# Performance work log

Hardware: AMD Instinct MI355X
Metric: run time of the kernel (lower is better)

Reference implementation:

```python
import jax, jax.numpy as jnp
import numpy as np

D_MODEL = 1024
N_HEADS = 16
D_K = D_MODEL // N_HEADS


def _xavier(key, shape):
    fan_in, fan_out = shape[1], shape[0]
    a = np.sqrt(6.0 / (fan_in + fan_out))
    return jax.random.uniform(key, shape, jnp.float32, -a, a)


def setup_inputs() -> dict:
    key = jax.random.key(0)
    kx, kq, kk, kv, ko = jax.random.split(key, 5)
    x = jax.random.normal(kx, (2, 2048, D_MODEL), jnp.float32)
    # nn.Linear weights are [out, in]; y = x @ W.T
    Wq = _xavier(kq, (D_MODEL, D_MODEL))
    Wk = _xavier(kk, (D_MODEL, D_MODEL))
    Wv = _xavier(kv, (D_MODEL, D_MODEL))
    Wo = _xavier(ko, (D_MODEL, D_MODEL))
    bo = jnp.zeros((D_MODEL,), jnp.float32)
    return {"x": x, "Wq": Wq, "Wk": Wk, "Wv": Wv, "Wo": Wo, "bo": bo}


def reference(x, Wq, Wk, Wv, Wo, bo):
    B, S, D = x.shape
    def split_heads(t):
        # [B,S,D] -> [B,H,S,d_k]
        return t.reshape(B, S, N_HEADS, D_K).transpose(0, 2, 1, 3)
    Q = split_heads(x @ Wq.T)
    K = split_heads(x @ Wk.T)
    V = split_heads(x @ Wv.T)
    scale = 1.0 / jnp.sqrt(jnp.asarray(D_K, x.dtype))
    scores = jnp.einsum('bhqd,bhkd->bhqk', Q, K) * scale  # [B,H,S,S]
    attn = jax.nn.softmax(scores, axis=-1)
    out = jnp.einsum('bhqk,bhkd->bhqd', attn, V)  # [B,H,S,d_k]
    out = out.transpose(0, 2, 1, 3).reshape(B, S, D)  # merge heads
    return out @ Wo.T + bo
```

## Files before the change

### kernel.cpp

```cpp
#include <hip/hip_runtime.h>


typedef __attribute__((ext_vector_type(8))) short bf16x8;
typedef __attribute__((ext_vector_type(4))) short bf16x4;
typedef __attribute__((ext_vector_type(4))) float f32x4;
typedef __attribute__((ext_vector_type(2))) unsigned int u32x2;

#define GK 1024
#define SEQ 2048
#define NHEAD 16
#define DKD 64
#define PADW 72

#define MFMA32(a, b, c) __builtin_amdgcn_mfma_f32_16x16x32_bf16((a), (b), (c), 0, 0, 0)
#define MFMA16(a, b, c) __builtin_amdgcn_mfma_f32_16x16x16bf16_1k((a), (b), (c), 0, 0, 0)

#if __has_builtin(__builtin_amdgcn_exp2f)
#define EXP2(x) __builtin_amdgcn_exp2f(x)
#else
#define EXP2(x) exp2f(x)
#endif

#define QSCALE 0.18033688011f

static __device__ __forceinline__ unsigned short f2bf(float f) {
    unsigned int u = __float_as_uint(f);
    u += 0x7fffu + ((u >> 16) & 1u);
    return (unsigned short)(u >> 16);
}

static __device__ __forceinline__ unsigned int pack_bf2(float a, float b) {
    unsigned int ua = __float_as_uint(a) + 0x8000u;
    unsigned int ub = __float_as_uint(b) + 0x8000u;
    return __builtin_amdgcn_perm(ub, ua, 0x07060302u);
}

__global__ __launch_bounds__(256) void cast_all(const float* __restrict__ x,
                                                const float* __restrict__ wq,
                                                const float* __restrict__ wk,
                                                const float* __restrict__ wv,
                                                const float* __restrict__ wo,
                                                unsigned short* __restrict__ Xb,
                                                unsigned short* __restrict__ Wqkv,
                                                unsigned short* __restrict__ Wob) {
    const int bid = blockIdx.x;
    const float* src; unsigned short* dst; int off;
    if (bid < 4096)      { src = x;  dst = Xb;             off = bid; }
    else if (bid < 5120) { src = wq; dst = Wqkv;           off = bid - 4096; }
    else if (bid < 6144) { src = wk; dst = Wqkv + 1048576; off = bid - 5120; }
    else if (bid < 7168) { src = wv; dst = Wqkv + 2097152; off = bid - 6144; }
    else                 { src = wo; dst = Wob;            off = bid - 7168; }
    const int i = off * 1024 + threadIdx.x * 4;
    float4 v = *(const float4*)(src + i);
    u32x2 p; p.x = pack_bf2(v.x, v.y); p.y = pack_bf2(v.z, v.w);
    *(u32x2*)(dst + i) = p;
}

template <int MODE, int BN>
__global__ __launch_bounds__(256) void gemm_bt(const unsigned short* __restrict__ A,
                                               const unsigned short* __restrict__ Bw,
                                               unsigned short* __restrict__ outb,
                                               float* __restrict__ outf,
                                               const float* __restrict__ bias) {
    constexpr int NJ = BN / 32;
    constexpr int LOOP_BYTES = 128 * 64 * 2 + BN * 64 * 2;
    constexpr int EPI_BYTES  = 4 * 64 * PADW * 2;
    constexpr int SMEM_BYTES = (MODE == 0)
        ? (LOOP_BYTES > EPI_BYTES ? LOOP_BYTES : EPI_BYTES)
        : LOOP_BYTES;
    __shared__ __align__(16) unsigned char SMEM[SMEM_BYTES];
    unsigned short* As = (unsigned short*)SMEM;
    unsigned short* Bs = As + 128 * 64;

    const int t    = threadIdx.x;
    const int lane = t & 63;
    const int w    = t >> 6;
    const int wm   = (w >> 1) * 64;
    const int wn   = (w & 1) * (BN / 2);
    const int bm0  = blockIdx.x * 128;
    const int bn0  = blockIdx.y * BN;
    const int lm   = lane & 15;
    const int lq   = lane >> 4;
    const int swzb = lm & 7;

    const unsigned short* Ab = A + (size_t)bm0 * GK;
    const unsigned short* Bb = Bw + (size_t)bn0 * GK;

    f32x4 acc[4][NJ];
    const f32x4 Z4 = {0.f, 0.f, 0.f, 0.f};
#pragma unroll
    for (int i = 0; i < 4; i++)
#pragma unroll
        for (int j = 0; j < NJ; j++) acc[i][j] = Z4;

    const int q_uni = (t & ~63);

    for (int k0 = 0; k0 < GK; k0 += 64) {
        __syncthreads();
#pragma unroll
        for (int i = 0; i < 4; ++i) {
            int q  = i * 256 + t;
            int r  = q >> 3;
            int gc = (q & 7) ^ (r & 7);
            int q0 = i * 256 + q_uni;
            __builtin_amdgcn_global_load_lds(
                (const __attribute__((address_space(1))) void*)(Ab + (size_t)r * GK + k0 + gc * 8),
                (__attribute__((address_space(3))) void*)(As + (size_t)q0 * 8),
                16, 0, 0);
        }
#pragma unroll
        for (int i = 0; i < BN / 32; ++i) {
            int q  = i * 256 + t;
            int r  = q >> 3;
            int gc = (q & 7) ^ (r & 7);
            int q0 = i * 256 + q_uni;
            __builtin_amdgcn_global_load_lds(
                (const __attribute__((address_space(1))) void*)(Bb + (size_t)r * GK + k0 + gc * 8),
                (__attribute__((address_space(3))) void*)(Bs + (size_t)q0 * 8),
                16, 0, 0);
        }
        __syncthreads();

#pragma unroll
        for (int kk = 0; kk < 2; ++kk) {
            const int swz = ((kk * 4 + lq) ^ swzb) * 8;
            bf16x8 af[4], bf[NJ];
#pragma unroll
            for (int i = 0; i < 4; i++)
                af[i] = *(const bf16x8*)(As + (wm + i * 16 + lm) * 64 + swz);
#pragma unroll
            for (int j = 0; j < NJ; j++)
                bf[j] = *(const bf16x8*)(Bs + (wn + j * 16 + lm) * 64 + swz);
#pragma unroll
            for (int i = 0; i < 4; i++)
#pragma unroll
                for (int j = 0; j < NJ; j++)
                    acc[i][j] = MFMA32(af[i], bf[j], acc[i][j]);
        }
    }

    if (MODE == 0) {
        __syncthreads();
        unsigned short* E  = (unsigned short*)SMEM;
        unsigned short* Ew = E + w * (64 * PADW);
        const int nbase = bn0 + wn;
        const int which = nbase >> 10;
        const int hh    = (nbase & 1023) >> 6;
        if (which != 2) {
            const float sc = (which == 0) ? QSCALE : 1.0f;
#pragma unroll
            for (int i = 0; i < 4; i++)
#pragma unroll
                for (int j = 0; j < 4; j++)
#pragma unroll
                    for (int r = 0; r < 4; r++)
                        Ew[(i * 16 + lq * 4 + r) * PADW + j * 16 + lm] =
                            f2bf(acc[i][j][r] * sc);
            unsigned short* dst = outb + (size_t)which * 4194304;
#pragma unroll
            for (int rep = 0; rep < 8; ++rep) {
                const int mm = rep * 8 + (lane >> 3);
                const int d0 = (lane & 7) * 8;
                uint4 v = *(const uint4*)(Ew + mm * PADW + d0);
                const int m_g = bm0 + wm + mm;
                const int b = m_g >> 11, s = m_g & 2047;
                *(uint4*)(dst + (((size_t)(b * NHEAD + hh)) * SEQ + s) * DKD + d0) = v;
            }
        } else {
#pragma unroll
            for (int i = 0; i < 4; i++)
#pragma unroll
                for (int j = 0; j < 4; j++) {
                    u32x2 pk;
                    pk.x = pack_bf2(acc[i][j][0], acc[i][j][1]);
                    pk.y = pack_bf2(acc[i][j][2], acc[i][j][3]);
                    *(u32x2*)(Ew + (j * 16 + lm) * PADW + i * 16 + lq * 4) = pk;
                }
            unsigned short* dst = outb + (size_t)2 * 4194304;
#pragma unroll
            for (int rep = 0; rep < 8; ++rep) {
                const int nn = rep * 8 + (lane >> 3);
                const int mc = (lane & 7) * 8;
                uint4 v = *(const uint4*)(Ew + nn * PADW + mc);
                const int m_g = bm0 + wm + mc;
                const int b = m_g >> 11, s0 = m_g & 2047;
                *(uint4*)(dst + (((size_t)(b * NHEAD + hh)) * DKD + nn) * SEQ + s0) = v;
            }
        }
    } else {
#pragma unroll
        for (int i = 0; i < 4; i++) {
            const int mbase = bm0 + wm + i * 16 + lq * 4;
#pragma unroll
            for (int j = 0; j < NJ; j++) {
                const int n = bn0 + wn + j * 16 + lm;
#pragma unroll
                for (int r = 0; r < 4; r++)
                    outf[(size_t)(mbase + r) * 1024 + n] = acc[i][j][r] + bias[n];
            }
        }
    }
}

__global__ __launch_bounds__(256, 3) void attn_kernel(const unsigned short* __restrict__ Qg,
                                                      const unsigned short* __restrict__ Kg,
                                                      const unsigned short* __restrict__ Vtg,
                                                      unsigned short* __restrict__ Og) {
    __shared__ __align__(16) unsigned short KV[2][2][64 * PADW];

    const int id  = blockIdx.x;
    const int xcd = id & 7;
    const int j8  = id >> 3;
    const int bh  = xcd * 4 + (j8 & 3);
    const int qb  = j8 >> 2;
    const unsigned short* Qp  = Qg  + ((size_t)bh * SEQ + qb * 64) * DKD;
    const unsigned short* Kp  = Kg  + (size_t)bh * SEQ * DKD;
    const unsigned short* Vtp = Vtg + (size_t)bh * DKD * SEQ;

    const int t    = threadIdx.x;
    const int lane = t & 63;
    const int w    = t >> 6;
    const int lm   = lane & 15;
    const int kq   = lane >> 4;

    const f32x4 Z4 = {0.f, 0.f, 0.f, 0.f};

    bf16x8 aq[4][2];
#pragma unroll
    for (int c = 0; c < 4; ++c)
#pragma unroll
        for (int kk = 0; kk < 2; ++kk)
            aq[c][kk] = *(const bf16x8*)(Qp + (size_t)(c * 16 + lm) * DKD + kk * 32 + kq * 8);

    f32x4 o[4][4];
    float ls[4];
#pragma unroll
    for (int c = 0; c < 4; ++c) {
        ls[c] = 0.f;
#pragma unroll
        for (int dj = 0; dj < 4; ++dj) o[c][dj] = Z4;
    }

    const int sr = t >> 2, sc = (t & 3) * 16;
    uint4 kreg0, kreg1, vreg0, vreg1;
    {
        const unsigned short* kp = Kp + (size_t)sr * DKD + sc;
        const unsigned short* vp = Vtp + (size_t)sr * SEQ + sc;
        uint4 a0 = *(const uint4*)(kp), a1 = *(const uint4*)(kp + 8);
        uint4 b0 = *(const uint4*)(vp), b1 = *(const uint4*)(vp + 8);
        uint4* dk = (uint4*)(&KV[0][0][sr * PADW + sc]); dk[0] = a0; dk[1] = a1;
        uint4* dv = (uint4*)(&KV[0][1][sr * PADW + sc]); dv[0] = b0; dv[1] = b1;
    }
    {
        const unsigned short* kp = Kp + (size_t)(64 + sr) * DKD + sc;
        kreg0 = *(const uint4*)(kp); kreg1 = *(const uint4*)(kp + 8);
        const unsigned short* vp = Vtp + (size_t)sr * SEQ + 64 + sc;
        vreg0 = *(const uint4*)(vp); vreg1 = *(const uint4*)(vp + 8);
    }

    for (int kt = 0; kt < 32; ++kt) {
        __syncthreads();
        if (kt + 1 < 32) {
            uint4* dk = (uint4*)(&KV[(kt + 1) & 1][0][sr * PADW + sc]);
            dk[0] = kreg0; dk[1] = kreg1;
            uint4* dv = (uint4*)(&KV[(kt + 1) & 1][1][sr * PADW + sc]);
            dv[0] = vreg0; dv[1] = vreg1;
        }
        if (kt + 2 < 32) {
            const unsigned short* kp = Kp + (size_t)((kt + 2) * 64 + sr) * DKD + sc;
            kreg0 = *(const uint4*)(kp); kreg1 = *(const uint4*)(kp + 8);
            const unsigned short* vp = Vtp + (size_t)sr * SEQ + (kt + 2) * 64 + sc;
            vreg0 = *(const uint4*)(vp); vreg1 = *(const uint4*)(vp + 8);
        }
        const unsigned short* Kc = &KV[kt & 1][0][0];
        const unsigned short* Vc = &KV[kt & 1][1][0];

        bf16x8 ak0 = *(const bf16x8*)(Kc + (w * 16 + lm) * PADW + kq * 8);
        bf16x8 ak1 = *(const bf16x8*)(Kc + (w * 16 + lm) * PADW + 32 + kq * 8);
        f32x4 s[4];
#pragma unroll
        for (int c = 0; c < 4; ++c) {
            s[c] = MFMA32(ak0, aq[c][0], Z4);
            s[c] = MFMA32(ak1, aq[c][1], s[c]);
        }

#pragma unroll
        for (int c = 0; c < 4; ++c) {
#pragma unroll
            for (int r = 0; r < 4; ++r) s[c][r] = EXP2(s[c][r]);
            ls[c] += (s[c][0] + s[c][1]) + (s[c][2] + s[c][3]);
        }

        bf16x4 ap[4];
#pragma unroll
        for (int c = 0; c < 4; ++c) {
            u32x2 pk;
            pk.x = pack_bf2(s[c][0], s[c][1]);
            pk.y = pack_bf2(s[c][2], s[c][3]);
            ap[c] = __builtin_bit_cast(bf16x4, pk);
        }

#pragma unroll
        for (int dj = 0; dj < 4; ++dj) {
            bf16x4 bv = *(const bf16x4*)(Vc + (dj * 16 + lm) * PADW + w * 16 + kq * 4);
#pragma unroll
            for (int c = 0; c < 4; ++c)
                o[c][dj] = MFMA16(ap[c], bv, o[c][dj]);
        }
    }

    __syncthreads();
    float* Lf = (float*)(&KV[0][0][0]);

#pragma unroll
    for (int c = 0; c < 4; ++c) {
        float v = ls[c];
        v += __shfl_xor(v, 16);
        v += __shfl_xor(v, 32);
        if (kq == 0) Lf[w * 64 + c * 16 + lm] = v;
    }
    __syncthreads();

    const int rq = t >> 2;
    const int dq = (t & 3) * 8;
    float li = (Lf[rq] + Lf[64 + rq]) + (Lf[128 + rq] + Lf[192 + rq]);
#if __has_builtin(__builtin_amdgcn_rcpf)
    li = __builtin_amdgcn_rcpf(li);
#else
    li = 1.0f / li;
#endif
    __syncthreads();

    const int b = bh >> 4, h = bh & 15;
#pragma unroll
    for (int p = 0; p < 2; ++p) {
#pragma unroll
        for (int c = 0; c < 4; ++c)
#pragma unroll
            for (int djh = 0; djh < 2; ++djh) {
                const int dj = 2 * p + djh;
#pragma unroll
                for (int r = 0; r < 4; ++r)
                    Lf[(w * 64 + c * 16 + kq * 4 + r) * 36 + djh * 16 + lm] = o[c][dj][r];
            }
        __syncthreads();
        f32x4 a0 = Z4, a1 = Z4;
#pragma unroll
        for (int wp = 0; wp < 4; ++wp) {
            a0 += *(const f32x4*)(Lf + (wp * 64 + rq) * 36 + dq);
            a1 += *(const f32x4*)(Lf + (wp * 64 + rq) * 36 + dq + 4);
        }
        uint4 outv;
        outv.x = pack_bf2(a0[0] * li, a0[1] * li);
        outv.y = pack_bf2(a0[2] * li, a0[3] * li);
        outv.z = pack_bf2(a1[0] * li, a1[1] * li);
        outv.w = pack_bf2(a1[2] * li, a1[3] * li);
        *(uint4*)(Og + (((size_t)(b * SEQ + qb * 64 + rq)) * NHEAD + h) * DKD + p * 32 + dq) = outv;
        __syncthreads();
    }
}

extern "C" void kernel_launch(void* const* d_in, const int* in_sizes, int n_in,
                              void* d_out, int out_size, void* d_ws, size_t ws_size,
                              hipStream_t stream) {
    const float* x  = (const float*)d_in[0];
    const float* Wq = (const float*)d_in[1];
    const float* Wk = (const float*)d_in[2];
    const float* Wv = (const float*)d_in[3];
    const float* Wo = (const float*)d_in[4];
    const float* bo = (const float*)d_in[5];
    float* out = (float*)d_out;

    unsigned short* ws = (unsigned short*)d_ws;
    unsigned short* Xb   = ws;
    unsigned short* Wqkv = ws + 4194304;
    unsigned short* Wob  = ws + 7340032;
    unsigned short* QKV  = ws + 8388608;
    unsigned short* Ob   = ws + 20971520;

    cast_all<<<8192, 256, 0, stream>>>(x, Wq, Wk, Wv, Wo, Xb, Wqkv, Wob);
    gemm_bt<0, 128><<<dim3(32, 24), 256, 0, stream>>>(Xb, Wqkv, QKV, nullptr, nullptr);
    attn_kernel<<<1024, 256, 0, stream>>>(QKV, QKV + 4194304, QKV + 8388608, Ob);
    gemm_bt<1, 64><<<dim3(32, 16), 256, 0, stream>>>(Ob, Wob, nullptr, out, bo);
}
```

Measured before the change: 190.5 us.

## Fuse fp32-to-bf16 cast of x into QKV GEMM with register prefetch

The separate cast of the activation x to bf16 is removed. The QKV GEMM now reads fp32 x directly, converts it to bf16 in registers, and stages it into LDS. Loading switches from async global_load_lds to register-prefetched loads for the next k-tile, which overlap with the MFMA work on the current tile. This removes a full write and re-read of the bf16 copy of x and one kernel's worth of blocks, but doubles the global bytes read for A per GEMM tile (re-read across 24 column blocks) and adds register pressure.

```diff
diff --git a/kernel.cpp b/kernel.cpp
--- a/kernel.cpp
+++ b/kernel.cpp
@@ -35,39 +35,30 @@
     return __builtin_amdgcn_perm(ub, ua, 0x07060302u);
 }
 
-__global__ __launch_bounds__(256) void cast_all(const float* __restrict__ x,
-                                                const float* __restrict__ wq,
-                                                const float* __restrict__ wk,
-                                                const float* __restrict__ wv,
-                                                const float* __restrict__ wo,
-                                                unsigned short* __restrict__ Xb,
-                                                unsigned short* __restrict__ Wqkv,
-                                                unsigned short* __restrict__ Wob) {
+__global__ __launch_bounds__(256) void cast_w(const float* __restrict__ wq,
+                                              const float* __restrict__ wk,
+                                              const float* __restrict__ wv,
+                                              const float* __restrict__ wo,
+                                              unsigned short* __restrict__ Wqkv,
+                                              unsigned short* __restrict__ Wob) {
     const int bid = blockIdx.x;
     const float* src; unsigned short* dst; int off;
-    if (bid < 4096)      { src = x;  dst = Xb;             off = bid; }
-    else if (bid < 5120) { src = wq; dst = Wqkv;           off = bid - 4096; }
-    else if (bid < 6144) { src = wk; dst = Wqkv + 1048576; off = bid - 5120; }
-    else if (bid < 7168) { src = wv; dst = Wqkv + 2097152; off = bid - 6144; }
-    else                 { src = wo; dst = Wob;            off = bid - 7168; }
+    if (bid < 1024)      { src = wq; dst = Wqkv;           off = bid; }
+    else if (bid < 2048) { src = wk; dst = Wqkv + 1048576; off = bid - 1024; }
+    else if (bid < 3072) { src = wv; dst = Wqkv + 2097152; off = bid - 2048; }
+    else                 { src = wo; dst = Wob;            off = bid - 3072; }
     const int i = off * 1024 + threadIdx.x * 4;
     float4 v = *(const float4*)(src + i);
     u32x2 p; p.x = pack_bf2(v.x, v.y); p.y = pack_bf2(v.z, v.w);
     *(u32x2*)(dst + i) = p;
 }
 
-template <int MODE, int BN>
-__global__ __launch_bounds__(256) void gemm_bt(const unsigned short* __restrict__ A,
-                                               const unsigned short* __restrict__ Bw,
-                                               unsigned short* __restrict__ outb,
-                                               float* __restrict__ outf,
-                                               const float* __restrict__ bias) {
-    constexpr int NJ = BN / 32;
-    constexpr int LOOP_BYTES = 128 * 64 * 2 + BN * 64 * 2;
+__global__ __launch_bounds__(256) void gemm_qkv(const float* __restrict__ X,
+                                                const unsigned short* __restrict__ Bw,
+                                                unsigned short* __restrict__ outb) {
+    constexpr int LOOP_BYTES = 128 * 64 * 2 * 2;
     constexpr int EPI_BYTES  = 4 * 64 * PADW * 2;
-    constexpr int SMEM_BYTES = (MODE == 0)
-        ? (LOOP_BYTES > EPI_BYTES ? LOOP_BYTES : EPI_BYTES)
-        : LOOP_BYTES;
+    constexpr int SMEM_BYTES = LOOP_BYTES > EPI_BYTES ? LOOP_BYTES : EPI_BYTES;
     __shared__ __align__(16) unsigned char SMEM[SMEM_BYTES];
     unsigned short* As = (unsigned short*)SMEM;
     unsigned short* Bs = As + 128 * 64;
@@ -76,22 +67,150 @@
     const int lane = t & 63;
     const int w    = t >> 6;
     const int wm   = (w >> 1) * 64;
-    const int wn   = (w & 1) * (BN / 2);
+    const int wn   = (w & 1) * 64;
     const int bm0  = blockIdx.x * 128;
-    const int bn0  = blockIdx.y * BN;
+    const int bn0  = blockIdx.y * 128;
     const int lm   = lane & 15;
     const int lq   = lane >> 4;
     const int swzb = lm & 7;
 
+    const int srow = t >> 3;
+    const int gc   = (t & 7) ^ (srow & 7);
+    const float*           Xa = X  + (size_t)(bm0 + srow) * GK + gc * 8;
+    const unsigned short*  Bb = Bw + (size_t)(bn0 + srow) * GK + gc * 8;
+
+    f32x4 acc[4][4];
+    const f32x4 Z4 = {0.f, 0.f, 0.f, 0.f};
+#pragma unroll
+    for (int i = 0; i < 4; i++)
+#pragma unroll
+        for (int j = 0; j < 4; j++) acc[i][j] = Z4;
+
+    uint4 pa[4], pb[4];
+#pragma unroll
+    for (int i = 0; i < 4; ++i) {
+        const float* xp = Xa + (size_t)i * 32 * GK;
+        float4 f0 = *(const float4*)(xp);
+        float4 f1 = *(const float4*)(xp + 4);
+        pa[i].x = pack_bf2(f0.x, f0.y); pa[i].y = pack_bf2(f0.z, f0.w);
+        pa[i].z = pack_bf2(f1.x, f1.y); pa[i].w = pack_bf2(f1.z, f1.w);
+        pb[i] = *(const uint4*)(Bb + (size_t)i * 32 * GK);
+    }
+
+    for (int kt = 0; kt < 16; ++kt) {
+        __syncthreads();
+#pragma unroll
+        for (int i = 0; i < 4; ++i) {
+            *(uint4*)(As + (size_t)(i * 256 + t) * 8) = pa[i];
+            *(uint4*)(Bs + (size_t)(i * 256 + t) * 8) = pb[i];
+        }
+        __syncthreads();
+        if (kt + 1 < 16) {
+            const int k0 = (kt + 1) * 64;
+#pragma unroll
+            for (int i = 0; i < 4; ++i) {
+                const float* xp = Xa + (size_t)i * 32 * GK + k0;
+                float4 f0 = *(const float4*)(xp);
+                float4 f1 = *(const float4*)(xp + 4);
+                pa[i].x = pack_bf2(f0.x, f0.y); pa[i].y = pack_bf2(f0.z, f0.w);
+                pa[i].z = pack_bf2(f1.x, f1.y); pa[i].w = pack_bf2(f1.z, f1.w);
+                pb[i] = *(const uint4*)(Bb + (size_t)i * 32 * GK + k0);
+            }
+        }
+#pragma unroll
+        for (int kk = 0; kk < 2; ++kk) {
+            const int swz = ((kk * 4 + lq) ^ swzb) * 8;
+            bf16x8 af[4], bf[4];
+#pragma unroll
+            for (int i = 0; i < 4; i++)
+                af[i] = *(const bf16x8*)(As + (wm + i * 16 + lm) * 64 + swz);
+#pragma unroll
+            for (int j = 0; j < 4; j++)
+                bf[j] = *(const bf16x8*)(Bs + (wn + j * 16 + lm) * 64 + swz);
+#pragma unroll
+            for (int i = 0; i < 4; i++)
+#pragma unroll
+                for (int j = 0; j < 4; j++)
+                    acc[i][j] = MFMA32(af[i], bf[j], acc[i][j]);
+        }
+    }
+
+    __syncthreads();
+    unsigned short* E  = (unsigned short*)SMEM;
+    unsigned short* Ew = E + w * (64 * PADW);
+    const int nbase = bn0 + wn;
+    const int which = nbase >> 10;
+    const int hh    = (nbase & 1023) >> 6;
+    if (which != 2) {
+        const float sc = (which == 0) ? QSCALE : 1.0f;
+#pragma unroll
+        for (int i = 0; i < 4; i++)
+#pragma unroll
+            for (int j = 0; j < 4; j++)
+#pragma unroll
+                for (int r = 0; r < 4; r++)
+                    Ew[(i * 16 + lq * 4 + r) * PADW + j * 16 + lm] =
+                        f2bf(acc[i][j][r] * sc);
+        unsigned short* dst = outb + (size_t)which * 4194304;
+#pragma unroll
+        for (int rep = 0; rep < 8; ++rep) {
+            const int mm = rep * 8 + (lane >> 3);
+            const int d0 = (lane & 7) * 8;
+            uint4 v = *(const uint4*)(Ew + mm * PADW + d0);
+            const int m_g = bm0 + wm + mm;
+            const int b = m_g >> 11, s = m_g & 2047;
+            *(uint4*)(dst + (((size_t)(b * NHEAD + hh)) * SEQ + s) * DKD + d0) = v;
+        }
+    } else {
+#pragma unroll
+        for (int i = 0; i < 4; i++)
+#pragma unroll
+            for (int j = 0; j < 4; j++) {
+                u32x2 pk;
+                pk.x = pack_bf2(acc[i][j][0], acc[i][j][1]);
+                pk.y = pack_bf2(acc[i][j][2], acc[i][j][3]);
+                *(u32x2*)(Ew + (j * 16 + lm) * PADW + i * 16 + lq * 4) = pk;
+            }
+        unsigned short* dst = outb + (size_t)2 * 4194304;
+#pragma unroll
+        for (int rep = 0; rep < 8; ++rep) {
+            const int nn = rep * 8 + (lane >> 3);
+            const int mc = (lane & 7) * 8;
+            uint4 v = *(const uint4*)(Ew + nn * PADW + mc);
+            const int m_g = bm0 + wm + mc;
+            const int b = m_g >> 11, s0 = m_g & 2047;
+            *(uint4*)(dst + (((size_t)(b * NHEAD + hh)) * DKD + nn) * SEQ + s0) = v;
+        }
+    }
+}
+
+__global__ __launch_bounds__(256) void gemm_proj(const unsigned short* __restrict__ A,
+                                                 const unsigned short* __restrict__ Bw,
+                                                 float* __restrict__ outf,
+                                                 const float* __restrict__ bias) {
+    __shared__ __align__(16) unsigned short As[128 * 64];
+    __shared__ __align__(16) unsigned short Bs[64 * 64];
+
+    const int t    = threadIdx.x;
+    const int lane = t & 63;
+    const int w    = t >> 6;
+    const int wm   = (w >> 1) * 64;
+    const int wn   = (w & 1) * 32;
+    const int bm0  = blockIdx.x * 128;
+    const int bn0  = blockIdx.y * 64;
+    const int lm   = lane & 15;
+    const int lq   = lane >> 4;
+    const int swzb = lm & 7;
+
     const unsigned short* Ab = A + (size_t)bm0 * GK;
     const unsigned short* Bb = Bw + (size_t)bn0 * GK;
 
-    f32x4 acc[4][NJ];
+    f32x4 acc[4][2];
     const f32x4 Z4 = {0.f, 0.f, 0.f, 0.f};
 #pragma unroll
     for (int i = 0; i < 4; i++)
 #pragma unroll
-        for (int j = 0; j < NJ; j++) acc[i][j] = Z4;
+        for (int j = 0; j < 2; j++) acc[i][j] = Z4;
 
     const int q_uni = (t & ~63);
 
@@ -99,23 +218,23 @@
         __syncthreads();
 #pragma unroll
         for (int i = 0; i < 4; ++i) {
-            int q  = i * 256 + t;
-            int r  = q >> 3;
-            int gc = (q & 7) ^ (r & 7);
-            int q0 = i * 256 + q_uni;
+            int q   = i * 256 + t;
+            int r   = q >> 3;
+            int gcs = (q & 7) ^ (r & 7);
+            int q0  = i * 256 + q_uni;
             __builtin_amdgcn_global_load_lds(
-                (const __attribute__((address_space(1))) void*)(Ab + (size_t)r * GK + k0 + gc * 8),
+                (const __attribute__((address_space(1))) void*)(Ab + (size_t)r * GK + k0 + gcs * 8),
                 (__attribute__((address_space(3))) void*)(As + (size_t)q0 * 8),
                 16, 0, 0);
         }
 #pragma unroll
-        for (int i = 0; i < BN / 32; ++i) {
-            int q  = i * 256 + t;
-            int r  = q >> 3;
-            int gc = (q & 7) ^ (r & 7);
-            int q0 = i * 256 + q_uni;
+        for (int i = 0; i < 2; ++i) {
+            int q   = i * 256 + t;
+            int r   = q >> 3;
+            int gcs = (q & 7) ^ (r & 7);
+            int q0  = i * 256 + q_uni;
             __builtin_amdgcn_global_load_lds(
-                (const __attribute__((address_space(1))) void*)(Bb + (size_t)r * GK + k0 + gc * 8),
+                (const __attribute__((address_space(1))) void*)(Bb + (size_t)r * GK + k0 + gcs * 8),
                 (__attribute__((address_space(3))) void*)(Bs + (size_t)q0 * 8),
                 16, 0, 0);
         }
@@ -124,80 +243,30 @@
 #pragma unroll
         for (int kk = 0; kk < 2; ++kk) {
             const int swz = ((kk * 4 + lq) ^ swzb) * 8;
-            bf16x8 af[4], bf[NJ];
+            bf16x8 af[4], bf[2];
 #pragma unroll
             for (int i = 0; i < 4; i++)
                 af[i] = *(const bf16x8*)(As + (wm + i * 16 + lm) * 64 + swz);
 #pragma unroll
-            for (int j = 0; j < NJ; j++)
+            for (int j = 0; j < 2; j++)
                 bf[j] = *(const bf16x8*)(Bs + (wn + j * 16 + lm) * 64 + swz);
 #pragma unroll
             for (int i = 0; i < 4; i++)
 #pragma unroll
-                for (int j = 0; j < NJ; j++)
+                for (int j = 0; j < 2; j++)
                     acc[i][j] = MFMA32(af[i], bf[j], acc[i][j]);
         }
     }
 
-    if (MODE == 0) {
-        __syncthreads();
-        unsigned short* E  = (unsigned short*)SMEM;
-        unsigned short* Ew = E + w * (64 * PADW);
-        const int nbase = bn0 + wn;
-        const int which = nbase >> 10;
-        const int hh    = (nbase & 1023) >> 6;
-        if (which != 2) {
-            const float sc = (which == 0) ? QSCALE : 1.0f;
-#pragma unroll
-            for (int i = 0; i < 4; i++)
-#pragma unroll
-                for (int j = 0; j < 4; j++)
-#pragma unroll
-                    for (int r = 0; r < 4; r++)
-                        Ew[(i * 16 + lq * 4 + r) * PADW + j * 16 + lm] =
-                            f2bf(acc[i][j][r] * sc);
-            unsigned short* dst = outb + (size_t)which * 4194304;
-#pragma unroll
-            for (int rep = 0; rep < 8; ++rep) {
-                const int mm = rep * 8 + (lane >> 3);
-                const int d0 = (lane & 7) * 8;
-                uint4 v = *(const uint4*)(Ew + mm * PADW + d0);
-                const int m_g = bm0 + wm + mm;
-                const int b = m_g >> 11, s = m_g & 2047;
-                *(uint4*)(dst + (((size_t)(b * NHEAD + hh)) * SEQ + s) * DKD + d0) = v;
-            }
-        } else {
-#pragma unroll
-            for (int i = 0; i < 4; i++)
-#pragma unroll
-                for (int j = 0; j < 4; j++) {
-                    u32x2 pk;
-                    pk.x = pack_bf2(acc[i][j][0], acc[i][j][1]);
-                    pk.y = pack_bf2(acc[i][j][2], acc[i][j][3]);
-                    *(u32x2*)(Ew + (j * 16 + lm) * PADW + i * 16 + lq * 4) = pk;
-                }
-            unsigned short* dst = outb + (size_t)2 * 4194304;
-#pragma unroll
-            for (int rep = 0; rep < 8; ++rep) {
-                const int nn = rep * 8 + (lane >> 3);
-                const int mc = (lane & 7) * 8;
-                uint4 v = *(const uint4*)(Ew + nn * PADW + mc);
-                const int m_g = bm0 + wm + mc;
-                const int b = m_g >> 11, s0 = m_g & 2047;
-                *(uint4*)(dst + (((size_t)(b * NHEAD + hh)) * DKD + nn) * SEQ + s0) = v;
-            }
-        }
-    } else {
-#pragma unroll
-        for (int i = 0; i < 4; i++) {
-            const int mbase = bm0 + wm + i * 16 + lq * 4;
-#pragma unroll
-            for (int j = 0; j < NJ; j++) {
-                const int n = bn0 + wn + j * 16 + lm;
-#pragma unroll
-                for (int r = 0; r < 4; r++)
-                    outf[(size_t)(mbase + r) * 1024 + n] = acc[i][j][r] + bias[n];
-            }
+#pragma unroll
+    for (int i = 0; i < 4; i++) {
+        const int mbase = bm0 + wm + i * 16 + lq * 4;
+#pragma unroll
+        for (int j = 0; j < 2; j++) {
+            const int n = bn0 + wn + j * 16 + lm;
+#pragma unroll
+            for (int r = 0; r < 4; r++)
+                outf[(size_t)(mbase + r) * 1024 + n] = acc[i][j][r] + bias[n];
         }
     }
 }
@@ -372,14 +441,13 @@
     float* out = (float*)d_out;
 
     unsigned short* ws = (unsigned short*)d_ws;
-    unsigned short* Xb   = ws;
     unsigned short* Wqkv = ws + 4194304;
     unsigned short* Wob  = ws + 7340032;
     unsigned short* QKV  = ws + 8388608;
     unsigned short* Ob   = ws + 20971520;
 
-    cast_all<<<8192, 256, 0, stream>>>(x, Wq, Wk, Wv, Wo, Xb, Wqkv, Wob);
-    gemm_bt<0, 128><<<dim3(32, 24), 256, 0, stream>>>(Xb, Wqkv, QKV, nullptr, nullptr);
+    cast_w<<<4096, 256, 0, stream>>>(Wq, Wk, Wv, Wo, Wqkv, Wob);
+    gemm_qkv<<<dim3(32, 24), 256, 0, stream>>>(x, Wqkv, QKV);
     attn_kernel<<<1024, 256, 0, stream>>>(QKV, QKV + 4194304, QKV + 8388608, Ob);
-    gemm_bt<1, 64><<<dim3(32, 16), 256, 0, stream>>>(Ob, Wob, nullptr, out, bo);
-}
+    gemm_proj<<<dim3(32, 16), 256, 0, stream>>>(Ob, Wob, out, bo);
+}
```

New measurement: 241.6 us. 26.8% more time.
